# Kernel optimization log

Hardware: AMD Instinct MI355X
Metric: run time of the kernel (lower is better)

## Reference

```python
import jax, jax.numpy as jnp
import numpy as np

B, S, D_MODEL, N_HEADS = 2, 2048, 2048, 16
D_K = D_MODEL // N_HEADS
MAX_SEQ_LEN = 4096


def _rope_tables(seq_len, d_k):
    # matches RotaryPositionalEmbedding buffers
    inv_freq = 1.0 / (10000.0 ** (jnp.arange(0, d_k, 2, dtype=jnp.float32) / d_k))
    pos = jnp.arange(seq_len, dtype=jnp.float32)
    freqs = pos[:, None] * inv_freq[None, :]  # [S, d_k/2]
    return jnp.cos(freqs), jnp.sin(freqs)


def _apply_rope(x, cos, sin):
    # x: [B, H, S, d_k]; cos/sin: [S, d_k/2] -> broadcast [1,1,S,d_k/2]
    cos = cos[None, None, :, :]
    sin = sin[None, None, :, :]
    x_even = x[..., ::2]
    x_odd = x[..., 1::2]
    r_even = x_even * cos - x_odd * sin
    r_odd = x_even * sin + x_odd * cos
    return jnp.stack([r_even, r_odd], axis=-1).reshape(x.shape)


def setup_inputs() -> dict:
    key = jax.random.key(0)
    ks = jax.random.split(key, 5)
    scale = 1.0 / np.sqrt(D_MODEL)
    return {
        "x": jax.random.normal(ks[0], (B, S, D_MODEL), jnp.float32),
        "wq_w": jax.random.normal(ks[1], (D_MODEL, D_MODEL), jnp.float32) * scale,
        "wq_b": jnp.zeros((D_MODEL,), jnp.float32),
        "wk_w": jax.random.normal(ks[2], (D_MODEL, D_MODEL), jnp.float32) * scale,
        "wk_b": jnp.zeros((D_MODEL,), jnp.float32),
        "wv_w": jax.random.normal(ks[3], (D_MODEL, D_MODEL), jnp.float32) * scale,
        "wv_b": jnp.zeros((D_MODEL,), jnp.float32),
        "wo_w": jax.random.normal(ks[4], (D_MODEL, D_MODEL), jnp.float32) * scale,
        "wo_b": jnp.zeros((D_MODEL,), jnp.float32),
    }


def reference(x, wq_w, wq_b, wk_w, wk_b, wv_w, wv_b, wo_w, wo_b):
    b, s, _ = x.shape
    # QKV projections (torch Linear: x @ W.T + b), split heads -> [B, H, S, d_k]
    def proj(w, bias):
        y = jnp.einsum('bsd,ed->bse', x, w) + bias
        return y.reshape(b, s, N_HEADS, D_K).transpose(0, 2, 1, 3)

    q = proj(wq_w, wq_b)
    k = proj(wk_w, wk_b)
    v = proj(wv_w, wv_b)

    cos, sin = _rope_tables(s, D_K)
    q = _apply_rope(q, cos, sin)
    k = _apply_rope(k, cos, sin)

    # causal SDPA
    scale = 1.0 / np.sqrt(D_K).astype(np.float32)
    scores = jnp.einsum('bhqd,bhkd->bhqk', q, k) * scale
    causal = jnp.tril(jnp.ones((s, s), dtype=bool))
    scores = jnp.where(causal[None, None, :, :], scores, jnp.float32(-jnp.inf))
    attn = jax.nn.softmax(scores, axis=-1)
    out = jnp.einsum('bhqk,bhkd->bhqd', attn, v)

    out = out.transpose(0, 2, 1, 3).reshape(b, s, D_MODEL)
    return jnp.einsum('bsd,ed->bse', out, wo_w) + wo_b
```

## Files before the change

kernel.cpp:

```cpp
#include <hip/hip_runtime.h>


#define DMODEL 2048
#define SEQ    2048
#define NHEAD  16
#define DKH    128
#define NBATCH 2
#define MTOK   (NBATCH*SEQ)

typedef float  f32x4  __attribute__((ext_vector_type(4)));
typedef __bf16 bf16x8 __attribute__((ext_vector_type(8)));
typedef unsigned short      u16;
typedef unsigned short      u16x4 __attribute__((ext_vector_type(4)));

#if __has_builtin(__builtin_amdgcn_exp2f)
#define EXP2F __builtin_amdgcn_exp2f
#else
#define EXP2F exp2f
#endif

__device__ __forceinline__ float b2f(u16 u) {
    union { unsigned i; float f; } x; x.i = ((unsigned)u) << 16; return x.f;
}
__device__ __forceinline__ u16 f2bf(float f) {
    union { float f; unsigned i; } x; x.f = f;
    unsigned r = x.i + 0x7fffu + ((x.i >> 16) & 1u);
    return (u16)(r >> 16);
}

__device__ __forceinline__ void load_lds16(const void* g, void* l) {
    __builtin_amdgcn_global_load_lds(
        (const __attribute__((address_space(1))) void*)g,
        (__attribute__((address_space(3))) void*)l, 16, 0, 0);
}

struct CastArgs {
    const float* src[5];
    u16*         dst[5];
    int          n4[5];
};
__global__ void cast_all_kernel(CastArgs a) {
    int j = blockIdx.y;
    int i = blockIdx.x * blockDim.x + threadIdx.x;
    if (i >= a.n4[j]) return;
    float4 f = ((const float4*)a.src[j])[i];
    uint2 o;
    o.x = (unsigned)f2bf(f.x) | ((unsigned)f2bf(f.y) << 16);
    o.y = (unsigned)f2bf(f.z) | ((unsigned)f2bf(f.w) << 16);
    ((uint2*)a.dst[j])[i] = o;
}

__global__ __launch_bounds__(256) void gemm_qkv(
    const u16* __restrict__ A, const u16* __restrict__ W,
    const float* __restrict__ qb, const float* __restrict__ kb,
    const float* __restrict__ vb,
    u16* __restrict__ QB, u16* __restrict__ KB, u16* __restrict__ VT)
{
    __shared__ u16 As[128 * 64];
    __shared__ u16 Bs[128 * 64];
    const int tid  = threadIdx.x;
    const int lane = tid & 63;
    const int w    = tid >> 6;
    const int wm   = w >> 1, wn = w & 1;
    const int quad = lane >> 4, l16 = lane & 15;
    const int row0 = blockIdx.y * 128;
    const int col0 = blockIdx.x * 128;
    const int K    = DMODEL;

    f32x4 acc[4][4] = {};

    for (int kt = 0; kt < K / 64; ++kt) {
        const int k0 = kt * 64;
#pragma unroll
        for (int i = 0; i < 4; ++i) {
            int cb = (i * 4 + w) * 64;
            int p  = cb + lane;
            int r  = p >> 3;
            int cl = (p & 7) ^ (r & 7);
            load_lds16(A + (size_t)(row0 + r) * K + k0 + cl * 8, (void*)(As + cb * 8));
            load_lds16(W + (size_t)(col0 + r) * K + k0 + cl * 8, (void*)(Bs + cb * 8));
        }
        __syncthreads();
#pragma unroll
        for (int ks = 0; ks < 2; ++ks) {
            bf16x8 af[4], bfr[4];
#pragma unroll
            for (int mi = 0; mi < 4; ++mi) {
                int r  = wm * 64 + mi * 16 + l16;
                int pc = (ks * 4 + quad) ^ (r & 7);
                af[mi] = *(const bf16x8*)(As + (r * 8 + pc) * 8);
            }
#pragma unroll
            for (int ni = 0; ni < 4; ++ni) {
                int r  = wn * 64 + ni * 16 + l16;
                int pc = (ks * 4 + quad) ^ (r & 7);
                bfr[ni] = *(const bf16x8*)(Bs + (r * 8 + pc) * 8);
            }
#pragma unroll
            for (int mi = 0; mi < 4; ++mi)
#pragma unroll
                for (int ni = 0; ni < 4; ++ni)
                    acc[mi][ni] = __builtin_amdgcn_mfma_f32_16x16x32_bf16(
                        af[mi], bfr[ni], acc[mi][ni], 0, 0, 0);
        }
        __syncthreads();
    }

    const int sect = col0 >> 11;
    if (sect == 2) {
#pragma unroll
        for (int mi = 0; mi < 4; ++mi) {
#pragma unroll
            for (int ni = 0; ni < 4; ++ni) {
                int colv = (col0 & 2047) + wn * 64 + ni * 16 + l16;
                float bv = vb[colv];
                int rowb = row0 + wm * 64 + mi * 16 + quad * 4;
                int bb = rowb >> 11, s = rowb & 2047;
                u16x4 pk;
#pragma unroll
                for (int r = 0; r < 4; ++r) pk[r] = f2bf(acc[mi][ni][r] + bv);
                *(u16x4*)(VT + (size_t)(bb * 2048 + colv) * 2048 + s) = pk;
            }
        }
    } else {
        const float* bias = sect ? kb : qb;
        u16* dst          = sect ? KB : QB;
#pragma unroll
        for (int mi = 0; mi < 4; ++mi) {
#pragma unroll
            for (int ni = 0; ni < 4; ++ni) {
                int col = (col0 & 2047) + wn * 64 + ni * 16 + l16;
                float bv = bias[col];
#pragma unroll
                for (int r = 0; r < 4; ++r) {
                    int row = row0 + wm * 64 + mi * 16 + quad * 4 + r;
                    dst[(size_t)row * 2048 + col] = f2bf(acc[mi][ni][r] + bv);
                }
            }
        }
    }
}

__global__ void rope_kernel(u16* __restrict__ Q, u16* __restrict__ Kt) {
    int idx = blockIdx.x * blockDim.x + threadIdx.x;
    u16* P      = blockIdx.y ? Kt : Q;
    float scale = blockIdx.y ? 1.0f : 0.12751743558f;
    int i   = idx & 63;
    int tok = idx >> 10;
    int s   = tok & (SEQ - 1);
    unsigned pr = *(const unsigned*)(P + 2 * (size_t)idx);
    float e = b2f((u16)(pr & 0xffff)), o = b2f((u16)(pr >> 16));
    float inv_freq = exp2f(-13.287712379549449f * (float)i * (1.0f / 64.0f));
    float ang = (float)s * inv_freq;
    float c, sn;
    sincosf(ang, &sn, &c);
    float re = (e * c - o * sn) * scale;
    float ro = (e * sn + o * c) * scale;
    *(unsigned*)(P + 2 * (size_t)idx) = (unsigned)f2bf(re) | ((unsigned)f2bf(ro) << 16);
}

__global__ __launch_bounds__(512, 4) void attn_kernel(
    const u16* __restrict__ Q, const u16* __restrict__ Kg,
    const u16* __restrict__ VTg, u16* __restrict__ Out)
{
    const int p  = blockIdx.x;
    const int bh = blockIdx.y;
    const int b  = bh >> 4, h = bh & 15;

    const int tid  = threadIdx.x;
    const int lane = tid & 63;
    const int w    = tid >> 6;
    const int half = w >> 2;
    const int wsub = w & 3;
    const int quad = lane >> 4, l16 = lane & 15;

    const int q_hi  = 31 - p;
    const int my_qt = half ? q_hi : p;
    const int q0    = my_qt * 64;

    __shared__ u16 Ks[64 * 128];
    __shared__ u16 Vt[128 * 64];
    __shared__ u16 Ps[8][16 * 72];

    bf16x8 qf[4];
    const u16* qrow = Q + (size_t)(b * SEQ + q0 + wsub * 16 + l16) * DMODEL + h * DKH;
#pragma unroll
    for (int ks = 0; ks < 4; ++ks) qf[ks] = *(const bf16x8*)(qrow + ks * 32 + quad * 8);

    f32x4 o[8] = {};
    float l_r[4] = { 0.f, 0.f, 0.f, 0.f };

    for (int kt = 0; kt <= q_hi; ++kt) {
        const int k0 = kt * 64;
#pragma unroll
        for (int i = 0; i < 2; ++i) {
            int cb = (i * 8 + w) * 64;
            int pc = cb + lane;
            int r  = pc >> 4;
            int cl = (pc & 15) ^ (r & 15);
            load_lds16(Kg + (size_t)(b * SEQ + k0 + r) * DMODEL + h * DKH + cl * 8,
                       (void*)(Ks + cb * 8));
        }
#pragma unroll
        for (int i = 0; i < 2; ++i) {
            int cb = (i * 8 + w) * 64;
            int pc = cb + lane;
            int r  = pc >> 3;
            int cl = (pc & 7) ^ (r & 7);
            load_lds16(VTg + (size_t)(b * 2048 + h * DKH + r) * SEQ + k0 + cl * 8,
                       (void*)(Vt + cb * 8));
        }
        __syncthreads();

        if (kt <= my_qt) {
            f32x4 sc[4] = {};
#pragma unroll
            for (int ks = 0; ks < 4; ++ks) {
#pragma unroll
                for (int nt = 0; nt < 4; ++nt) {
                    int r  = nt * 16 + l16;
                    int pc = (ks * 4 + quad) ^ (r & 15);
                    bf16x8 kf = *(const bf16x8*)(Ks + (r * 16 + pc) * 8);
                    sc[nt] = __builtin_amdgcn_mfma_f32_16x16x32_bf16(qf[ks], kf, sc[nt], 0, 0, 0);
                }
            }
            if (kt == my_qt) {
#pragma unroll
                for (int nt = 0; nt < 4; ++nt)
#pragma unroll
                    for (int r = 0; r < 4; ++r) {
                        int col = k0 + nt * 16 + l16;
                        int row = q0 + wsub * 16 + quad * 4 + r;
                        if (col > row) sc[nt][r] = -1e30f;
                    }
            }
#pragma unroll
            for (int nt = 0; nt < 4; ++nt)
#pragma unroll
                for (int r = 0; r < 4; ++r) {
                    float pv = EXP2F(sc[nt][r] - 32.0f);
                    l_r[r] += pv;
                    Ps[w][(quad * 4 + r) * 72 + nt * 16 + l16] = f2bf(pv);
                }
#pragma unroll
            for (int ks = 0; ks < 2; ++ks) {
                bf16x8 pf = *(const bf16x8*)(&Ps[w][l16 * 72 + ks * 32 + quad * 8]);
#pragma unroll
                for (int nt = 0; nt < 8; ++nt) {
                    int r  = nt * 16 + l16;
                    int pc = (ks * 4 + quad) ^ (r & 7);
                    bf16x8 vf = *(const bf16x8*)(Vt + r * 64 + pc * 8);
                    o[nt] = __builtin_amdgcn_mfma_f32_16x16x32_bf16(pf, vf, o[nt], 0, 0, 0);
                }
            }
        }
        __syncthreads();
    }

#pragma unroll
    for (int r = 0; r < 4; ++r) {
#pragma unroll
        for (int off = 1; off < 16; off <<= 1) l_r[r] += __shfl_xor(l_r[r], off);
        float inv = 1.0f / l_r[r];
        int row = q0 + wsub * 16 + quad * 4 + r;
#pragma unroll
        for (int nt = 0; nt < 8; ++nt)
            Out[(size_t)(b * SEQ + row) * DMODEL + h * DKH + nt * 16 + l16] = f2bf(o[nt][r] * inv);
    }
}

__global__ __launch_bounds__(256) void gemm_o(
    const u16* __restrict__ A, const u16* __restrict__ W,
    const float* __restrict__ bias, float* __restrict__ Cout,
    int M, int N, int K)
{
    __shared__ u16 As[128 * 64];
    __shared__ u16 Bs[128 * 64];
    const int tid  = threadIdx.x;
    const int lane = tid & 63;
    const int w    = tid >> 6;
    const int wm   = w >> 1, wn = w & 1;
    const int quad = lane >> 4, l16 = lane & 15;
    const int row0 = blockIdx.y * 128;
    const int col0 = blockIdx.x * 128;

    f32x4 acc[4][4] = {};

    for (int kt = 0; kt < K / 64; ++kt) {
        const int k0 = kt * 64;
#pragma unroll
        for (int i = 0; i < 4; ++i) {
            int cb = (i * 4 + w) * 64;
            int p  = cb + lane;
            int r  = p >> 3;
            int cl = (p & 7) ^ (r & 7);
            load_lds16(A + (size_t)(row0 + r) * K + k0 + cl * 8, (void*)(As + cb * 8));
            load_lds16(W + (size_t)(col0 + r) * K + k0 + cl * 8, (void*)(Bs + cb * 8));
        }
        __syncthreads();
#pragma unroll
        for (int ks = 0; ks < 2; ++ks) {
            bf16x8 af[4], bfr[4];
#pragma unroll
            for (int mi = 0; mi < 4; ++mi) {
                int r  = wm * 64 + mi * 16 + l16;
                int pc = (ks * 4 + quad) ^ (r & 7);
                af[mi] = *(const bf16x8*)(As + (r * 8 + pc) * 8);
            }
#pragma unroll
            for (int ni = 0; ni < 4; ++ni) {
                int r  = wn * 64 + ni * 16 + l16;
                int pc = (ks * 4 + quad) ^ (r & 7);
                bfr[ni] = *(const bf16x8*)(Bs + (r * 8 + pc) * 8);
            }
#pragma unroll
            for (int mi = 0; mi < 4; ++mi)
#pragma unroll
                for (int ni = 0; ni < 4; ++ni)
                    acc[mi][ni] = __builtin_amdgcn_mfma_f32_16x16x32_bf16(
                        af[mi], bfr[ni], acc[mi][ni], 0, 0, 0);
        }
        __syncthreads();
    }
#pragma unroll
    for (int mi = 0; mi < 4; ++mi) {
#pragma unroll
        for (int ni = 0; ni < 4; ++ni) {
            int col = col0 + wn * 64 + ni * 16 + l16;
            float bv = bias[col];
#pragma unroll
            for (int r = 0; r < 4; ++r) {
                int row = row0 + wm * 64 + mi * 16 + quad * 4 + r;
                Cout[(size_t)row * N + col] = acc[mi][ni][r] + bv;
            }
        }
    }
}

extern "C" void kernel_launch(void* const* d_in, const int* in_sizes, int n_in,
                              void* d_out, int out_size, void* d_ws, size_t ws_size,
                              hipStream_t stream)
{
    const float* x    = (const float*)d_in[0];
    const float* wq_w = (const float*)d_in[1];
    const float* wq_b = (const float*)d_in[2];
    const float* wk_w = (const float*)d_in[3];
    const float* wk_b = (const float*)d_in[4];
    const float* wv_w = (const float*)d_in[5];
    const float* wv_b = (const float*)d_in[6];
    const float* wo_w = (const float*)d_in[7];
    const float* wo_b = (const float*)d_in[8];
    float* out = (float*)d_out;

    char* ws = (char*)d_ws;
    u16* XB   = (u16*)(ws);
    u16* WQKV = (u16*)(ws + (16u << 20));
    u16* WOB  = (u16*)(ws + (40u << 20));
    u16* QB   = (u16*)(ws + (48u << 20));
    u16* KB   = (u16*)(ws + (64u << 20));
    u16* VTB  = (u16*)(ws + (80u << 20));

    CastArgs ca;
    ca.src[0] = x;    ca.dst[0] = XB;                         ca.n4[0] = (MTOK * DMODEL) / 4;
    ca.src[1] = wq_w; ca.dst[1] = WQKV;                       ca.n4[1] = (DMODEL * DMODEL) / 4;
    ca.src[2] = wk_w; ca.dst[2] = WQKV + DMODEL * DMODEL;     ca.n4[2] = (DMODEL * DMODEL) / 4;
    ca.src[3] = wv_w; ca.dst[3] = WQKV + 2 * DMODEL * DMODEL; ca.n4[3] = (DMODEL * DMODEL) / 4;
    ca.src[4] = wo_w; ca.dst[4] = WOB;                        ca.n4[4] = (DMODEL * DMODEL) / 4;
    cast_all_kernel<<<dim3(8192, 5), 256, 0, stream>>>(ca);

    gemm_qkv<<<dim3(48, 32), 256, 0, stream>>>(XB, WQKV, wq_b, wk_b, wv_b, QB, KB, VTB);

    rope_kernel<<<dim3((MTOK * NHEAD * 64) / 256, 2), 256, 0, stream>>>(QB, KB);

    attn_kernel<<<dim3(16, NBATCH * NHEAD), 512, 0, stream>>>(QB, KB, VTB, XB);

    gemm_o<<<dim3(16, 32), 256, 0, stream>>>(XB, WOB, wo_b, out, MTOK, DMODEL, DMODEL);
}
```

Measured before the change: 392.6 us.

## Replace GEMMs with 4-stage LDS-pipelined 128x256 kernel with XCD-aware block remap

Result: slower. 457.9 us (+16.6%).

```diff
diff --git a/kernel.cpp b/kernel.cpp
--- a/kernel.cpp
+++ b/kernel.cpp
@@ -32,6 +32,15 @@
     __builtin_amdgcn_global_load_lds(
         (const __attribute__((address_space(1))) void*)g,
         (__attribute__((address_space(3))) void*)l, 16, 0, 0);
+}
+
+#define WAITVM(N) asm volatile("s_waitcnt vmcnt(" #N ")" ::: "memory")
+
+__device__ __forceinline__ void pipe_barrier() {
+    __builtin_amdgcn_sched_barrier(0);
+    __builtin_amdgcn_s_barrier();
+    __builtin_amdgcn_sched_barrier(0);
+    asm volatile("" ::: "memory");
 }
 
 struct CastArgs {
@@ -50,91 +59,133 @@
     ((uint2*)a.dst[j])[i] = o;
 }
 
-__global__ __launch_bounds__(256) void gemm_qkv(
+template<int MODE>
+__global__ __launch_bounds__(512, 2) void gemm_pipe(
     const u16* __restrict__ A, const u16* __restrict__ W,
     const float* __restrict__ qb, const float* __restrict__ kb,
     const float* __restrict__ vb,
-    u16* __restrict__ QB, u16* __restrict__ KB, u16* __restrict__ VT)
+    u16* __restrict__ QB, u16* __restrict__ KB, u16* __restrict__ VT,
+    float* __restrict__ FO)
 {
-    __shared__ u16 As[128 * 64];
-    __shared__ u16 Bs[128 * 64];
+    constexpr int NTM = 32;
+    constexpr int NWG = MODE ? 256 : 768;
+    constexpr int NT  = 64;
+
+    __shared__ __align__(16) u16 As[4][128 * 32];
+    __shared__ __align__(16) u16 Bs[4][256 * 32];
+
     const int tid  = threadIdx.x;
     const int lane = tid & 63;
     const int w    = tid >> 6;
-    const int wm   = w >> 1, wn = w & 1;
+    const int wm   = w >> 2, wn = w & 3;
     const int quad = lane >> 4, l16 = lane & 15;
-    const int row0 = blockIdx.y * 128;
-    const int col0 = blockIdx.x * 128;
-    const int K    = DMODEL;
+
+    const int nb   = (blockIdx.x & 7) * (NWG >> 3) + (blockIdx.x >> 3);
+    const int row0 = (nb % NTM) * 128;
+    const int col0 = (nb / NTM) * 256;
 
     f32x4 acc[4][4] = {};
 
-    for (int kt = 0; kt < K / 64; ++kt) {
-        const int k0 = kt * 64;
-#pragma unroll
-        for (int i = 0; i < 4; ++i) {
-            int cb = (i * 4 + w) * 64;
-            int p  = cb + lane;
-            int r  = p >> 3;
-            int cl = (p & 7) ^ (r & 7);
-            load_lds16(A + (size_t)(row0 + r) * K + k0 + cl * 8, (void*)(As + cb * 8));
-            load_lds16(W + (size_t)(col0 + r) * K + k0 + cl * 8, (void*)(Bs + cb * 8));
-        }
-        __syncthreads();
-#pragma unroll
-        for (int ks = 0; ks < 2; ++ks) {
-            bf16x8 af[4], bfr[4];
-#pragma unroll
-            for (int mi = 0; mi < 4; ++mi) {
-                int r  = wm * 64 + mi * 16 + l16;
-                int pc = (ks * 4 + quad) ^ (r & 7);
-                af[mi] = *(const bf16x8*)(As + (r * 8 + pc) * 8);
-            }
+    auto stage = [&](int t) {
+        const int k0 = t * 32;
+        u16* Asl = As[t & 3];
+        u16* Bsl = Bs[t & 3];
+        {
+            int p = tid, r = p >> 2;
+            int c = (p & 3) ^ ((r >> 1) & 3);
+            load_lds16(A + (size_t)(row0 + r) * DMODEL + k0 + c * 8,
+                       (void*)(Asl + w * 512));
+        }
+#pragma unroll
+        for (int i = 0; i < 2; ++i) {
+            int p = i * 512 + tid, r = p >> 2;
+            int c = (p & 3) ^ ((r >> 1) & 3);
+            load_lds16(W + (size_t)(col0 + r) * DMODEL + k0 + c * 8,
+                       (void*)(Bsl + (i * 8 + w) * 512));
+        }
+    };
+
+    auto compute = [&](int t) {
+        const u16* Asl = As[t & 3];
+        const u16* Bsl = Bs[t & 3];
+        bf16x8 af[4], bfr[4];
+#pragma unroll
+        for (int mi = 0; mi < 4; ++mi) {
+            int ra = wm * 64 + mi * 16 + l16;
+            af[mi] = *(const bf16x8*)(Asl + (ra * 4 + (quad ^ ((ra >> 1) & 3))) * 8);
+        }
+#pragma unroll
+        for (int ni = 0; ni < 4; ++ni) {
+            int rb = wn * 64 + ni * 16 + l16;
+            bfr[ni] = *(const bf16x8*)(Bsl + (rb * 4 + (quad ^ ((rb >> 1) & 3))) * 8);
+        }
+        __builtin_amdgcn_s_setprio(1);
+#pragma unroll
+        for (int mi = 0; mi < 4; ++mi)
+#pragma unroll
+            for (int ni = 0; ni < 4; ++ni)
+                acc[mi][ni] = __builtin_amdgcn_mfma_f32_16x16x32_bf16(
+                    af[mi], bfr[ni], acc[mi][ni], 0, 0, 0);
+        __builtin_amdgcn_s_setprio(0);
+    };
+
+    stage(0); stage(1); stage(2);
+
+    for (int t = 0; t < NT - 3; ++t) {
+        WAITVM(6);
+        pipe_barrier();
+        stage(t + 3);
+        compute(t);
+    }
+    WAITVM(6); pipe_barrier(); compute(NT - 3);
+    WAITVM(3); pipe_barrier(); compute(NT - 2);
+    WAITVM(0); pipe_barrier(); compute(NT - 1);
+
+    if constexpr (MODE == 1) {
+#pragma unroll
+        for (int mi = 0; mi < 4; ++mi) {
 #pragma unroll
             for (int ni = 0; ni < 4; ++ni) {
-                int r  = wn * 64 + ni * 16 + l16;
-                int pc = (ks * 4 + quad) ^ (r & 7);
-                bfr[ni] = *(const bf16x8*)(Bs + (r * 8 + pc) * 8);
-            }
-#pragma unroll
-            for (int mi = 0; mi < 4; ++mi)
-#pragma unroll
-                for (int ni = 0; ni < 4; ++ni)
-                    acc[mi][ni] = __builtin_amdgcn_mfma_f32_16x16x32_bf16(
-                        af[mi], bfr[ni], acc[mi][ni], 0, 0, 0);
-        }
-        __syncthreads();
-    }
-
-    const int sect = col0 >> 11;
-    if (sect == 2) {
-#pragma unroll
-        for (int mi = 0; mi < 4; ++mi) {
-#pragma unroll
-            for (int ni = 0; ni < 4; ++ni) {
-                int colv = (col0 & 2047) + wn * 64 + ni * 16 + l16;
-                float bv = vb[colv];
-                int rowb = row0 + wm * 64 + mi * 16 + quad * 4;
-                int bb = rowb >> 11, s = rowb & 2047;
-                u16x4 pk;
-#pragma unroll
-                for (int r = 0; r < 4; ++r) pk[r] = f2bf(acc[mi][ni][r] + bv);
-                *(u16x4*)(VT + (size_t)(bb * 2048 + colv) * 2048 + s) = pk;
-            }
-        }
-    } else {
-        const float* bias = sect ? kb : qb;
-        u16* dst          = sect ? KB : QB;
-#pragma unroll
-        for (int mi = 0; mi < 4; ++mi) {
-#pragma unroll
-            for (int ni = 0; ni < 4; ++ni) {
-                int col = (col0 & 2047) + wn * 64 + ni * 16 + l16;
-                float bv = bias[col];
+                int col = col0 + wn * 64 + ni * 16 + l16;
+                float bv = qb[col];
 #pragma unroll
                 for (int r = 0; r < 4; ++r) {
                     int row = row0 + wm * 64 + mi * 16 + quad * 4 + r;
-                    dst[(size_t)row * 2048 + col] = f2bf(acc[mi][ni][r] + bv);
+                    FO[(size_t)row * DMODEL + col] = acc[mi][ni][r] + bv;
+                }
+            }
+        }
+    } else {
+        const int sect = col0 >> 11;
+        if (sect == 2) {
+#pragma unroll
+            for (int mi = 0; mi < 4; ++mi) {
+#pragma unroll
+                for (int ni = 0; ni < 4; ++ni) {
+                    int colv = (col0 & 2047) + wn * 64 + ni * 16 + l16;
+                    float bv = vb[colv];
+                    int rowb = row0 + wm * 64 + mi * 16 + quad * 4;
+                    int bb = rowb >> 11, s = rowb & 2047;
+                    u16x4 pk;
+#pragma unroll
+                    for (int r = 0; r < 4; ++r) pk[r] = f2bf(acc[mi][ni][r] + bv);
+                    *(u16x4*)(VT + (size_t)(bb * 2048 + colv) * 2048 + s) = pk;
+                }
+            }
+        } else {
+            const float* bias = sect ? kb : qb;
+            u16* dst          = sect ? KB : QB;
+#pragma unroll
+            for (int mi = 0; mi < 4; ++mi) {
+#pragma unroll
+                for (int ni = 0; ni < 4; ++ni) {
+                    int col = (col0 & 2047) + wn * 64 + ni * 16 + l16;
+                    float bv = bias[col];
+#pragma unroll
+                    for (int r = 0; r < 4; ++r) {
+                        int row = row0 + wm * 64 + mi * 16 + quad * 4 + r;
+                        dst[(size_t)row * 2048 + col] = f2bf(acc[mi][ni][r] + bv);
+                    }
                 }
             }
         }
@@ -269,74 +320,6 @@
     }
 }
 
-__global__ __launch_bounds__(256) void gemm_o(
-    const u16* __restrict__ A, const u16* __restrict__ W,
-    const float* __restrict__ bias, float* __restrict__ Cout,
-    int M, int N, int K)
-{
-    __shared__ u16 As[128 * 64];
-    __shared__ u16 Bs[128 * 64];
-    const int tid  = threadIdx.x;
-    const int lane = tid & 63;
-    const int w    = tid >> 6;
-    const int wm   = w >> 1, wn = w & 1;
-    const int quad = lane >> 4, l16 = lane & 15;
-    const int row0 = blockIdx.y * 128;
-    const int col0 = blockIdx.x * 128;
-
-    f32x4 acc[4][4] = {};
-
-    for (int kt = 0; kt < K / 64; ++kt) {
-        const int k0 = kt * 64;
-#pragma unroll
-        for (int i = 0; i < 4; ++i) {
-            int cb = (i * 4 + w) * 64;
-            int p  = cb + lane;
-            int r  = p >> 3;
-            int cl = (p & 7) ^ (r & 7);
-            load_lds16(A + (size_t)(row0 + r) * K + k0 + cl * 8, (void*)(As + cb * 8));
-            load_lds16(W + (size_t)(col0 + r) * K + k0 + cl * 8, (void*)(Bs + cb * 8));
-        }
-        __syncthreads();
-#pragma unroll
-        for (int ks = 0; ks < 2; ++ks) {
-            bf16x8 af[4], bfr[4];
-#pragma unroll
-            for (int mi = 0; mi < 4; ++mi) {
-                int r  = wm * 64 + mi * 16 + l16;
-                int pc = (ks * 4 + quad) ^ (r & 7);
-                af[mi] = *(const bf16x8*)(As + (r * 8 + pc) * 8);
-            }
-#pragma unroll
-            for (int ni = 0; ni < 4; ++ni) {
-                int r  = wn * 64 + ni * 16 + l16;
-                int pc = (ks * 4 + quad) ^ (r & 7);
-                bfr[ni] = *(const bf16x8*)(Bs + (r * 8 + pc) * 8);
-            }
-#pragma unroll
-            for (int mi = 0; mi < 4; ++mi)
-#pragma unroll
-                for (int ni = 0; ni < 4; ++ni)
-                    acc[mi][ni] = __builtin_amdgcn_mfma_f32_16x16x32_bf16(
-                        af[mi], bfr[ni], acc[mi][ni], 0, 0, 0);
-        }
-        __syncthreads();
-    }
-#pragma unroll
-    for (int mi = 0; mi < 4; ++mi) {
-#pragma unroll
-        for (int ni = 0; ni < 4; ++ni) {
-            int col = col0 + wn * 64 + ni * 16 + l16;
-            float bv = bias[col];
-#pragma unroll
-            for (int r = 0; r < 4; ++r) {
-                int row = row0 + wm * 64 + mi * 16 + quad * 4 + r;
-                Cout[(size_t)row * N + col] = acc[mi][ni][r] + bv;
-            }
-        }
-    }
-}
-
 extern "C" void kernel_launch(void* const* d_in, const int* in_sizes, int n_in,
                               void* d_out, int out_size, void* d_ws, size_t ws_size,
                               hipStream_t stream)
@@ -368,11 +351,13 @@
     ca.src[4] = wo_w; ca.dst[4] = WOB;                        ca.n4[4] = (DMODEL * DMODEL) / 4;
     cast_all_kernel<<<dim3(8192, 5), 256, 0, stream>>>(ca);
 
-    gemm_qkv<<<dim3(48, 32), 256, 0, stream>>>(XB, WQKV, wq_b, wk_b, wv_b, QB, KB, VTB);
+    gemm_pipe<0><<<dim3(768), 512, 0, stream>>>(
+        XB, WQKV, wq_b, wk_b, wv_b, QB, KB, VTB, nullptr);
 
     rope_kernel<<<dim3((MTOK * NHEAD * 64) / 256, 2), 256, 0, stream>>>(QB, KB);
 
     attn_kernel<<<dim3(16, NBATCH * NHEAD), 512, 0, stream>>>(QB, KB, VTB, XB);
 
-    gemm_o<<<dim3(16, 32), 256, 0, stream>>>(XB, WOB, wo_b, out, MTOK, DMODEL, DMODEL);
-}
+    gemm_pipe<1><<<dim3(256), 512, 0, stream>>>(
+        XB, WOB, wo_b, nullptr, nullptr, nullptr, nullptr, nullptr, out);
+}
```
